# Performance work log

Hardware: AMD Instinct MI355X
Metric: run time of the kernel (lower is better)

Reference implementation:

```python
import jax, jax.numpy as jnp
import numpy as np

K = 1024
H = 16
B = 2
T = 2048


def setup_inputs() -> dict:
    key = jax.random.key(0)
    ks = jax.random.split(key, 8)
    x = jax.random.normal(ks[0], (B, T, K), dtype=jnp.float32)
    mask = jax.random.randint(ks[1], (B, T), 0, 2, dtype=jnp.int32)
    scale = 1.0 / np.sqrt(K)
    Wk = jax.random.normal(ks[2], (K, K), dtype=jnp.float32) * scale
    Wq = jax.random.normal(ks[3], (K, K), dtype=jnp.float32) * scale
    Wv = jax.random.normal(ks[4], (K, K), dtype=jnp.float32) * scale
    Wu = jax.random.normal(ks[5], (K, K), dtype=jnp.float32) * scale
    bu = jnp.zeros((K,), dtype=jnp.float32)
    return {"x": x, "mask": mask, "Wk": Wk, "Wq": Wq, "Wv": Wv, "Wu": Wu, "bu": bu}


def reference(x, mask, Wk, Wq, Wv, Wu, bu):
    b, t, k = x.shape
    h = H
    s = k // h
    # Linear(k, k, bias=False): y = x @ W.T
    keys = (x @ Wk.T).reshape(b, t, h, s)
    queries = (x @ Wq.T).reshape(b, t, h, s)
    values = (x @ Wv.T).reshape(b, t, h, s)
    # raw scores [b, h, t, t]; NOTE: original applies NO 1/sqrt(s) scaling
    raw = jnp.einsum("bqhd,bkhd->bhqk", queries, keys)
    # mask [b, t] broadcast over heads and query positions (keys masked)
    raw = jnp.where(mask[:, None, None, :] == 0, -jnp.inf, raw)
    weights = jax.nn.softmax(raw, axis=-1)
    ys = jnp.einsum("bhqk,bkhd->bqhd", weights, values).reshape(b, t, k)
    return ys @ Wu.T + bu
```

## Files before the change

### kernel.cpp

```cpp
#include <hip/hip_runtime.h>
#include <hip/hip_bf16.h>
#include <math.h>

#define TS 2048
#define KD 1024
#define NH 16
#define SD 64
#define MB 4096
#define LOG2E 1.4426950408889634f

typedef __attribute__((ext_vector_type(8))) short bf16x8;
typedef __attribute__((ext_vector_type(4))) short bf16x4;
typedef __attribute__((ext_vector_type(4))) float f32x4;
typedef unsigned short ushort_t;

#define MFMA32(a, b, c) __builtin_amdgcn_mfma_f32_16x16x32_bf16(a, b, c, 0, 0, 0)

union frag8 { bf16x8 v8; bf16x4 h[2]; };

__device__ __forceinline__ ushort_t f2bf_rn(float f) {
    union { __hip_bfloat16 h; ushort_t u; } c;
    c.h = __float2bfloat16(f);
    return c.u;
}
__device__ __forceinline__ float bf2f(ushort_t u) {
    union { unsigned u; float f; } v; v.u = ((unsigned)u) << 16;
    return v.f;
}
__device__ __forceinline__ ushort4 pk4_bf(float a, float b, float c, float d) {
    union { __hip_bfloat162 h; ushort2 u; } x, y;
    x.h = __float22bfloat162_rn(make_float2(a, b));
    y.h = __float22bfloat162_rn(make_float2(c, d));
    return make_ushort4(x.u.x, x.u.y, y.u.x, y.u.y);
}
__device__ __forceinline__ void gload_lds16(const void* g, void* l) {
    __builtin_amdgcn_global_load_lds(
        (const __attribute__((address_space(1))) unsigned int*)g,
        (__attribute__((address_space(3))) unsigned int*)l, 16, 0, 0);
}

__global__ __launch_bounds__(256)
void conv_all(const float* __restrict__ x, const float* __restrict__ wq,
              const float* __restrict__ wk, const float* __restrict__ wv,
              const float* __restrict__ wu,
              ushort_t* XH, ushort_t* XL, ushort_t* WqH, ushort_t* WqL,
              ushort_t* WkH, ushort_t* WkL, ushort_t* WvH, ushort_t* WuH)
{
    int z = blockIdx.y;
    const float* src; ushort_t* H; ushort_t* L = nullptr; int nblk;
    switch (z) {
        case 0:  src = x;  H = XH;  L = XL;  nblk = 4096; break;
        case 1:  src = wq; H = WqH; L = WqL; nblk = 1024; break;
        case 2:  src = wk; H = WkH; L = WkL; nblk = 1024; break;
        case 3:  src = wv; H = WvH;          nblk = 1024; break;
        default: src = wu; H = WuH;          nblk = 1024; break;
    }
    if ((int)blockIdx.x >= nblk) return;
    int idx = blockIdx.x * 256 + threadIdx.x;
    float4 v = ((const float4*)src)[idx];
    if (z == 1) { v.x *= LOG2E; v.y *= LOG2E; v.z *= LOG2E; v.w *= LOG2E; }
    ushort_t h0 = f2bf_rn(v.x), h1 = f2bf_rn(v.y);
    ushort_t h2 = f2bf_rn(v.z), h3 = f2bf_rn(v.w);
    ((ushort4*)H)[idx] = make_ushort4(h0, h1, h2, h3);
    if (L) {
        ushort_t l0 = f2bf_rn(v.x - bf2f(h0)), l1 = f2bf_rn(v.y - bf2f(h1));
        ushort_t l2 = f2bf_rn(v.z - bf2f(h2)), l3 = f2bf_rn(v.w - bf2f(h3));
        ((ushort4*)L)[idx] = make_ushort4(l0, l1, l2, l3);
    }
}

__global__ __launch_bounds__(256)
void gemm_bf16(const ushort_t* __restrict__ Ah, const ushort_t* __restrict__ Al,
               const ushort_t* __restrict__ Bqh, const ushort_t* __restrict__ Bql,
               const ushort_t* __restrict__ Bkh, const ushort_t* __restrict__ Bkl,
               const ushort_t* __restrict__ Bvh, const ushort_t* __restrict__ Buh,
               ushort_t* __restrict__ OQh, ushort_t* __restrict__ OQl,
               ushort_t* __restrict__ OKh, ushort_t* __restrict__ OKl,
               ushort_t* __restrict__ OVt, float* __restrict__ OF,
               const float* __restrict__ bias, int epi_base)
{
    const int epi = epi_base + blockIdx.z;
    const ushort_t* Bh; const ushort_t* Bl = nullptr;
    if      (epi == 0) { Bh = Bqh; Bl = Bql; }
    else if (epi == 1) { Bh = Bkh; Bl = Bkl; }
    else if (epi == 2) { Bh = Bvh; }
    else               { Bh = Buh; }
    const bool terms3 = (epi < 2);

    __shared__ ushort_t sAh[64 * 32];
    __shared__ ushort_t sAl[64 * 32];
    __shared__ ushort_t sBh[128 * 32];
    __shared__ ushort_t sBl[128 * 32];

    const int tid = threadIdx.x;
    const int wave = tid >> 6, lane = tid & 63;
    const int col = lane & 15, quad = lane >> 4;
    const int wm = wave >> 1, wn = wave & 1;
    const int m0 = blockIdx.y * 64, n0 = blockIdx.x * 128;

    f32x4 acc[2][4];
#pragma unroll
    for (int i = 0; i < 2; ++i)
#pragma unroll
        for (int j = 0; j < 4; ++j) acc[i][j] = (f32x4){0.f, 0.f, 0.f, 0.f};

    for (int k0 = 0; k0 < KD; k0 += 32) {
        {
            int row = tid >> 2, k8 = tid & 3;
            int lo  = wave * 64 * 8;
            gload_lds16(Ah + (size_t)(m0 + row) * KD + k0 + k8 * 8, sAh + lo);
            if (terms3)
                gload_lds16(Al + (size_t)(m0 + row) * KD + k0 + k8 * 8, sAl + lo);
        }
#pragma unroll
        for (int j = 0; j < 2; ++j) {
            int s   = wave * 128 + j * 64 + lane;
            int row = s >> 2, k8 = s & 3;
            int lo  = (wave * 128 + j * 64) * 8;
            gload_lds16(Bh + (size_t)(n0 + row) * KD + k0 + k8 * 8, sBh + lo);
            if (terms3)
                gload_lds16(Bl + (size_t)(n0 + row) * KD + k0 + k8 * 8, sBl + lo);
        }
        __syncthreads();

        bf16x8 fbh[4], fbl[4];
#pragma unroll
        for (int j = 0; j < 4; ++j) {
            int r = (wn * 64 + j * 16 + col) * 32 + quad * 8;
            fbh[j] = *(const bf16x8*)&sBh[r];
            if (terms3) fbl[j] = *(const bf16x8*)&sBl[r];
        }
#pragma unroll
        for (int i = 0; i < 2; ++i) {
            int r = (wm * 32 + i * 16 + col) * 32 + quad * 8;
            bf16x8 fah = *(const bf16x8*)&sAh[r];
            if (terms3) {
                bf16x8 fal = *(const bf16x8*)&sAl[r];
#pragma unroll
                for (int j = 0; j < 4; ++j) {
                    acc[i][j] = MFMA32(fah, fbh[j], acc[i][j]);
                    acc[i][j] = MFMA32(fah, fbl[j], acc[i][j]);
                    acc[i][j] = MFMA32(fal, fbh[j], acc[i][j]);
                }
            } else {
#pragma unroll
                for (int j = 0; j < 4; ++j)
                    acc[i][j] = MFMA32(fah, fbh[j], acc[i][j]);
            }
        }
        __syncthreads();
    }

    if (epi <= 1) {
        ushort_t* OH = (epi == 0) ? OQh : OKh;
        ushort_t* OL = (epi == 0) ? OQl : OKl;
#pragma unroll
        for (int i = 0; i < 2; ++i) {
            int m = m0 + wm * 32 + i * 16 + quad * 4;
#pragma unroll
            for (int j = 0; j < 4; ++j) {
                int n = n0 + wn * 64 + j * 16 + col;
#pragma unroll
                for (int r = 0; r < 4; ++r) {
                    float v = acc[i][j][r];
                    ushort_t hv = f2bf_rn(v);
                    size_t off = (size_t)(m + r) * KD + n;
                    OH[off] = hv;
                    OL[off] = f2bf_rn(v - bf2f(hv));
                }
            }
        }
    } else if (epi == 2) {
#pragma unroll
        for (int i = 0; i < 2; ++i) {
            int m = m0 + wm * 32 + i * 16 + quad * 4;
            int bb = m >> 11, t = m & (TS - 1);
#pragma unroll
            for (int j = 0; j < 4; ++j) {
                int n = n0 + wn * 64 + j * 16 + col;
                int hh = n >> 6, d = n & 63;
                ushort4 pk = pk4_bf(acc[i][j][0], acc[i][j][1], acc[i][j][2], acc[i][j][3]);
                *(ushort4*)(OVt + ((size_t)(bb * NH + hh) * SD + d) * TS + t) = pk;
            }
        }
    } else {
#pragma unroll
        for (int i = 0; i < 2; ++i) {
            int m = m0 + wm * 32 + i * 16 + quad * 4;
#pragma unroll
            for (int j = 0; j < 4; ++j) {
                int n = n0 + wn * 64 + j * 16 + col;
                float bj = bias[n];
#pragma unroll
                for (int r = 0; r < 4; ++r)
                    OF[(size_t)(m + r) * KD + n] = acc[i][j][r] + bj;
            }
        }
    }
}

__global__ __launch_bounds__(256, 2)
void attn_mfma(const ushort_t* __restrict__ QH, const ushort_t* __restrict__ QL,
               const ushort_t* __restrict__ KH, const ushort_t* __restrict__ KL,
               const ushort_t* __restrict__ VT, const int* __restrict__ mask,
               ushort_t* __restrict__ YH)
{
    const int qt = blockIdx.x;
    const int h  = blockIdx.y;
    const int b  = blockIdx.z;
    const int bh = b * NH + h;

    const int tid  = threadIdx.x;
    const int wave = tid >> 6;
    const int lane = tid & 63;
    const int col  = lane & 15;
    const int quad = lane >> 4;

    __shared__ ushort_t smem[12288];
    ushort_t* sKH = smem;
    ushort_t* sKL = smem + 4096;
    ushort_t* sVT = smem + 8192;
    __shared__ float lred[4][64];

    bf16x8 bqh[4][2], bql[4][2];
#pragma unroll
    for (int qf = 0; qf < 4; ++qf) {
        size_t qrow = (size_t)(b * TS + qt * 64 + qf * 16 + col) * KD + h * SD;
#pragma unroll
        for (int c = 0; c < 2; ++c) {
            bqh[qf][c] = *(const bf16x8*)(QH + qrow + c * 32 + quad * 8);
            bql[qf][c] = *(const bf16x8*)(QL + qrow + c * 32 + quad * 8);
        }
    }

    const int l8 = lane >> 3, l7 = lane & 7;
    const ushort_t* gp[6];
    ushort_t* ld[6];
#pragma unroll
    for (int r = 0; r < 6; ++r) {
        int cc  = (r & 1) * 4 + wave;
        int row = cc * 8 + l8;
        int gs  = l7 ^ (row & 7);
        if (r < 2)      gp[r] = KH + (size_t)(b * TS + row) * KD + h * SD + gs * 8;
        else if (r < 4) gp[r] = KL + (size_t)(b * TS + row) * KD + h * SD + gs * 8;
        else            gp[r] = VT + ((size_t)bh * SD + row) * TS + gs * 8;
        ld[r] = ((r < 2) ? sKH : (r < 4) ? sKL : sVT) + cc * 512;
    }
    const int* mp = mask + b * TS + wave * 16 + quad * 4;

    float lp[4] = {0.f, 0.f, 0.f, 0.f};
    f32x4 O[4][4];
#pragma unroll
    for (int dt = 0; dt < 4; ++dt)
#pragma unroll
        for (int qf = 0; qf < 4; ++qf) O[dt][qf] = (f32x4){0.f, 0.f, 0.f, 0.f};

    frag8 av[4], bp4[4];
#pragma unroll
    for (int i = 0; i < 4; ++i) {
        av[i].v8  = (bf16x8){0, 0, 0, 0, 0, 0, 0, 0};
        bp4[i].v8 = (bf16x8){0, 0, 0, 0, 0, 0, 0, 0};
    }

    for (int kt = 0; kt < TS / 64; ++kt) {
#pragma unroll
        for (int r = 0; r < 6; ++r) gload_lds16(gp[r], ld[r]);
        int4 mv = *(const int4*)mp;
        mp += 64;
#pragma unroll
        for (int r = 0; r < 6; ++r) gp[r] += (r < 4) ? 64 * KD : 64;
        __syncthreads();

        f32x4 sinit;
        sinit[0] = mv.x ? 0.f : -INFINITY;
        sinit[1] = mv.y ? 0.f : -INFINITY;
        sinit[2] = mv.z ? 0.f : -INFINITY;
        sinit[3] = mv.w ? 0.f : -INFINITY;

        bf16x8 akh[2], akl[2];
#pragma unroll
        for (int c = 0; c < 2; ++c) {
            int sl = (c * 4 + quad) ^ (col & 7);
            akh[c] = *(const bf16x8*)&sKH[((wave * 16 + col) * 8 + sl) * 8];
            akl[c] = *(const bf16x8*)&sKL[((wave * 16 + col) * 8 + sl) * 8];
        }
#pragma unroll
        for (int dt = 0; dt < 4; ++dt) {
            int sl = (wave * 2 + (quad >> 1)) ^ (col & 7);
            av[dt].h[0] = *(const bf16x4*)&sVT[((dt * 16 + col) * 8 + sl) * 8 + (quad & 1) * 4];
        }

#pragma unroll
        for (int qf = 0; qf < 4; ++qf) {
            f32x4 s1 = sinit;
            f32x4 s2 = (f32x4){0.f, 0.f, 0.f, 0.f};
            s1 = MFMA32(akh[0], bqh[qf][0], s1);
            s2 = MFMA32(akl[0], bqh[qf][0], s2);
            s2 = MFMA32(akh[0], bql[qf][0], s2);
            s1 = MFMA32(akh[1], bqh[qf][1], s1);
            s2 = MFMA32(akl[1], bqh[qf][1], s2);
            s2 = MFMA32(akh[1], bql[qf][1], s2);
            float p0 = exp2f(s1[0] + s2[0]);
            float p1 = exp2f(s1[1] + s2[1]);
            float p2 = exp2f(s1[2] + s2[2]);
            float p3 = exp2f(s1[3] + s2[3]);
            lp[qf] += (p0 + p1) + (p2 + p3);
            union { ushort4 u4; bf16x4 v4; } pk;
            pk.u4 = pk4_bf(p0, p1, p2, p3);
            bp4[qf].h[0] = pk.v4;
        }

#pragma unroll
        for (int dt = 0; dt < 4; ++dt)
#pragma unroll
            for (int qf = 0; qf < 4; ++qf)
                O[dt][qf] = MFMA32(av[dt].v8, bp4[qf].v8, O[dt][qf]);

        __syncthreads();
    }

#pragma unroll
    for (int qf = 0; qf < 4; ++qf) {
        float v = lp[qf];
        v += __shfl_xor(v, 16);
        v += __shfl_xor(v, 32);
        if (lane < 16) lred[wave][qf * 16 + lane] = v;
    }

    float* Of = (float*)smem;
#pragma unroll
    for (int w = 1; w < 4; ++w) {
        __syncthreads();
        if (wave == w) {
#pragma unroll
            for (int dt = 0; dt < 4; ++dt)
#pragma unroll
                for (int qf = 0; qf < 4; ++qf)
                    *(f32x4*)&Of[((dt * 4 + qf) * 64 + lane) * 4] = O[dt][qf];
        }
        __syncthreads();
        if (wave == 0) {
#pragma unroll
            for (int dt = 0; dt < 4; ++dt)
#pragma unroll
                for (int qf = 0; qf < 4; ++qf)
                    O[dt][qf] += *(const f32x4*)&Of[((dt * 4 + qf) * 64 + lane) * 4];
        }
    }
    if (wave == 0) {
        float linv[4];
#pragma unroll
        for (int qf = 0; qf < 4; ++qf) {
            int q = qf * 16 + col;
            linv[qf] = 1.f / (lred[0][q] + lred[1][q] + lred[2][q] + lred[3][q]);
        }
#pragma unroll
        for (int dt = 0; dt < 4; ++dt)
#pragma unroll
            for (int qf = 0; qf < 4; ++qf) {
                ushort4 pk = pk4_bf(O[dt][qf][0] * linv[qf], O[dt][qf][1] * linv[qf],
                                    O[dt][qf][2] * linv[qf], O[dt][qf][3] * linv[qf]);
                *(ushort4*)(YH + (size_t)(b * TS + qt * 64 + qf * 16 + col) * KD +
                            h * SD + dt * 16 + quad * 4) = pk;
            }
    }
}

extern "C" void kernel_launch(void* const* d_in, const int* in_sizes, int n_in,
                              void* d_out, int out_size, void* d_ws, size_t ws_size,
                              hipStream_t stream) {
    const float* x    = (const float*)d_in[0];
    const int*   mask = (const int*)d_in[1];
    const float* Wk   = (const float*)d_in[2];
    const float* Wq   = (const float*)d_in[3];
    const float* Wv   = (const float*)d_in[4];
    const float* Wu   = (const float*)d_in[5];
    const float* bu   = (const float*)d_in[6];
    float* out = (float*)d_out;

    char* w = (char*)d_ws;
    const size_t M1 = (size_t)1 << 20;
    ushort_t* XH  = (ushort_t*)(w);
    ushort_t* XL  = (ushort_t*)(w + 8  * M1);
    ushort_t* WqH = (ushort_t*)(w + 16 * M1);
    ushort_t* WqL = (ushort_t*)(w + 18 * M1);
    ushort_t* WkH = (ushort_t*)(w + 20 * M1);
    ushort_t* WkL = (ushort_t*)(w + 22 * M1);
    ushort_t* WvH = (ushort_t*)(w + 24 * M1);
    ushort_t* QHb = (ushort_t*)(w + 26 * M1);
    ushort_t* QLb = (ushort_t*)(w + 34 * M1);
    ushort_t* KHb = (ushort_t*)(w + 42 * M1);
    ushort_t* KLb = (ushort_t*)(w + 50 * M1);
    ushort_t* WuH = (ushort_t*)(w + 58 * M1);
    ushort_t* VTb = (ushort_t*)d_out;
    ushort_t* YHb = (ushort_t*)(w);

    dim3 blk(256);
    conv_all<<<dim3(4096, 5), blk, 0, stream>>>(x, Wq, Wk, Wv, Wu,
                                                XH, XL, WqH, WqL, WkH, WkL, WvH, WuH);
    gemm_bf16<<<dim3(8, 64, 3), blk, 0, stream>>>(XH, XL, WqH, WqL, WkH, WkL, WvH, WuH,
                                                  QHb, QLb, KHb, KLb, VTb, nullptr,
                                                  nullptr, 0);
    attn_mfma<<<dim3(32, NH, 2), blk, 0, stream>>>(QHb, QLb, KHb, KLb, VTb, mask, YHb);
    gemm_bf16<<<dim3(8, 64, 1), blk, 0, stream>>>(YHb, nullptr, WqH, WqL, WkH, WkL, WvH, WuH,
                                                  nullptr, nullptr, nullptr, nullptr, nullptr,
                                                  out, bu, 3);
}
```

Baseline: 303.6 us.

## Load K/V fragments directly from global memory, dropping LDS staging and barriers

Each wave now loads its K-high, K-low and V^T MFMA fragments straight from global memory into registers instead of staging the tiles through shared memory with async global-to-LDS copies. Because no wave reads another wave's slice, both per-iteration __syncthreads barriers go away, and the shared buffer shrinks to just the reduction scratch. The trade-off is that loads are no longer staged ahead through LDS, so each iteration waits on global-memory latency. Access patterns also change: the V^T reads become 8-byte strided loads across rows of length TS.

Result: slower. 326.5 us (+7.6%).

```diff
diff --git a/kernel.cpp b/kernel.cpp
--- a/kernel.cpp
+++ b/kernel.cpp
@@ -216,10 +216,7 @@
     const int col  = lane & 15;
     const int quad = lane >> 4;
 
-    __shared__ ushort_t smem[12288];
-    ushort_t* sKH = smem;
-    ushort_t* sKL = smem + 4096;
-    ushort_t* sVT = smem + 8192;
+    __shared__ float Of[4096];
     __shared__ float lred[4][64];
 
     bf16x8 bqh[4][2], bql[4][2];
@@ -233,20 +230,10 @@
         }
     }
 
-    const int l8 = lane >> 3, l7 = lane & 7;
-    const ushort_t* gp[6];
-    ushort_t* ld[6];
-#pragma unroll
-    for (int r = 0; r < 6; ++r) {
-        int cc  = (r & 1) * 4 + wave;
-        int row = cc * 8 + l8;
-        int gs  = l7 ^ (row & 7);
-        if (r < 2)      gp[r] = KH + (size_t)(b * TS + row) * KD + h * SD + gs * 8;
-        else if (r < 4) gp[r] = KL + (size_t)(b * TS + row) * KD + h * SD + gs * 8;
-        else            gp[r] = VT + ((size_t)bh * SD + row) * TS + gs * 8;
-        ld[r] = ((r < 2) ? sKH : (r < 4) ? sKL : sVT) + cc * 512;
-    }
-    const int* mp = mask + b * TS + wave * 16 + quad * 4;
+    const ushort_t* kh_p = KH + (size_t)(b * TS + wave * 16 + col) * KD + h * SD + quad * 8;
+    const ushort_t* kl_p = KL + (size_t)(b * TS + wave * 16 + col) * KD + h * SD + quad * 8;
+    const ushort_t* vt_p = VT + ((size_t)bh * SD + col) * TS + wave * 16 + quad * 4;
+    const int*      mp   = mask + b * TS + wave * 16 + quad * 4;
 
     float lp[4] = {0.f, 0.f, 0.f, 0.f};
     f32x4 O[4][4];
@@ -263,32 +250,22 @@
     }
 
     for (int kt = 0; kt < TS / 64; ++kt) {
-#pragma unroll
-        for (int r = 0; r < 6; ++r) gload_lds16(gp[r], ld[r]);
+        bf16x8 akh[2], akl[2];
+        akh[0] = *(const bf16x8*)(kh_p);
+        akh[1] = *(const bf16x8*)(kh_p + 32);
+        akl[0] = *(const bf16x8*)(kl_p);
+        akl[1] = *(const bf16x8*)(kl_p + 32);
+#pragma unroll
+        for (int dt = 0; dt < 4; ++dt)
+            av[dt].h[0] = *(const bf16x4*)(vt_p + (size_t)(dt * 16) * TS);
         int4 mv = *(const int4*)mp;
-        mp += 64;
-#pragma unroll
-        for (int r = 0; r < 6; ++r) gp[r] += (r < 4) ? 64 * KD : 64;
-        __syncthreads();
+        kh_p += 64 * KD; kl_p += 64 * KD; vt_p += 64; mp += 64;
 
         f32x4 sinit;
         sinit[0] = mv.x ? 0.f : -INFINITY;
         sinit[1] = mv.y ? 0.f : -INFINITY;
         sinit[2] = mv.z ? 0.f : -INFINITY;
         sinit[3] = mv.w ? 0.f : -INFINITY;
-
-        bf16x8 akh[2], akl[2];
-#pragma unroll
-        for (int c = 0; c < 2; ++c) {
-            int sl = (c * 4 + quad) ^ (col & 7);
-            akh[c] = *(const bf16x8*)&sKH[((wave * 16 + col) * 8 + sl) * 8];
-            akl[c] = *(const bf16x8*)&sKL[((wave * 16 + col) * 8 + sl) * 8];
-        }
-#pragma unroll
-        for (int dt = 0; dt < 4; ++dt) {
-            int sl = (wave * 2 + (quad >> 1)) ^ (col & 7);
-            av[dt].h[0] = *(const bf16x4*)&sVT[((dt * 16 + col) * 8 + sl) * 8 + (quad & 1) * 4];
-        }
 
 #pragma unroll
         for (int qf = 0; qf < 4; ++qf) {
@@ -315,8 +292,6 @@
 #pragma unroll
             for (int qf = 0; qf < 4; ++qf)
                 O[dt][qf] = MFMA32(av[dt].v8, bp4[qf].v8, O[dt][qf]);
-
-        __syncthreads();
     }
 
 #pragma unroll
@@ -327,7 +302,6 @@
         if (lane < 16) lred[wave][qf * 16 + lane] = v;
     }
 
-    float* Of = (float*)smem;
 #pragma unroll
     for (int w = 1; w < 4; ++w) {
         __syncthreads();
```
